# Kernel optimization log

Measured on AMD Instinct MI355X. Metric: run time of the kernel, lower is better.

## Reference

```python
import jax, jax.numpy as jnp
import numpy as np

NUM_NODES = 100000
NUM_EDGES = 1600000
NUM_GRAPHS = 64
NUM_FEATURES = 128
DIM = 128
OUTPUT_SIZE = 16


def setup_inputs() -> dict:
    key = jax.random.key(0)
    ks = jax.random.split(key, 7)
    features = jax.random.normal(ks[0], (NUM_NODES, NUM_FEATURES), dtype=jnp.float32)
    W1 = jax.random.normal(ks[1], (NUM_FEATURES, DIM), dtype=jnp.float32) / np.sqrt(NUM_FEATURES)
    W2 = jax.random.normal(ks[2], (DIM, DIM), dtype=jnp.float32) / np.sqrt(DIM)
    W3 = jax.random.normal(ks[3], (DIM, OUTPUT_SIZE), dtype=jnp.float32) / np.sqrt(DIM)
    src = jax.random.randint(ks[4], (NUM_EDGES,), 0, NUM_NODES, dtype=jnp.int32)
    dst = jax.random.randint(ks[5], (NUM_EDGES,), 0, NUM_NODES, dtype=jnp.int32)
    graph_ids = jnp.sort(jax.random.randint(ks[6], (NUM_NODES,), 0, NUM_GRAPHS, dtype=jnp.int32))
    return {"features": features, "W1": W1, "W2": W2, "W3": W3,
            "src": src, "dst": dst, "graph_ids": graph_ids}


def _graph_conv(x, W, src, dst, num_nodes):
    # DGL GraphConv, norm='none', bias=False: h_v = sum_{u -> v} (x_u @ W)
    xw = x @ W                      # [N, dim]
    msg = xw[src]                   # gather per edge [E, dim]
    return jax.ops.segment_sum(msg, dst, num_segments=num_nodes)


def reference(features, W1, W2, W3, src, dst, graph_ids):
    n = features.shape[0]
    h = jax.nn.relu(_graph_conv(features, W1, src, dst, n))  # conv1 + ReLU
    h = _graph_conv(h, W2, src, dst, n)                      # conv2
    # dgl.mean_nodes: per-graph mean over nodes
    sums = jax.ops.segment_sum(h, graph_ids, num_segments=NUM_GRAPHS)          # [G, dim]
    counts = jax.ops.segment_sum(jnp.ones((n,), h.dtype), graph_ids,
                                 num_segments=NUM_GRAPHS)                       # [G]
    pooled = sums / jnp.maximum(counts, 1.0)[:, None]
    out = pooled @ W3                                         # fc1 (no bias)
    return jax.nn.sigmoid(out)                                # torch.sigmoid activation
```

## Files before the change

### kernel.cpp

```cpp
#include <hip/hip_runtime.h>

#define FNX 4
#define CSLOT 32
#define OVCAP 65536
#define AP_CHUNK 32
#define AP_GBINS 8

typedef short bf16x8 __attribute__((ext_vector_type(8)));
typedef float f32x4  __attribute__((ext_vector_type(4)));

union U4S8 { uint4 u; bf16x8 s; };

__device__ __forceinline__ unsigned int f2bf(float f) {
    unsigned int u = __float_as_uint(f);
    return (u + 0x7fffu + ((u >> 16) & 1u)) >> 16;
}

__device__ __forceinline__ f32x4 nt_ld_f4(const float4* p) {
    return __builtin_nontemporal_load((const f32x4*)p);
}

__device__ __forceinline__ unsigned int enc_u8(float f) {
    return (unsigned int)fminf(fmaxf(f + 0.5f, 0.f), 255.9f);
}

__global__ __launch_bounds__(256) void fconv(
    const float4* __restrict__ F4, uint4* __restrict__ B4, int n16)
{
    int t = blockIdx.x * 256 + threadIdx.x;
    if (t >= n16) return;
    f32x4 a = nt_ld_f4(&F4[4 * t + 0]);
    f32x4 b = nt_ld_f4(&F4[4 * t + 1]);
    f32x4 c = nt_ld_f4(&F4[4 * t + 2]);
    f32x4 d = nt_ld_f4(&F4[4 * t + 3]);
    uint4 o;
    #define P4(v) (enc_u8(v.x * 16.f + 128.f) | (enc_u8(v.y * 16.f + 128.f) << 8) | \
                   (enc_u8(v.z * 16.f + 128.f) << 16) | (enc_u8(v.w * 16.f + 128.f) << 24))
    o.x = P4(a); o.y = P4(b); o.z = P4(c); o.w = P4(d);
    #undef P4
    B4[t] = o;
}

__global__ __launch_bounds__(256) void fillfix_xcd(
    const int* __restrict__ src, const int* __restrict__ dst,
    int* __restrict__ cnt, int* __restrict__ col,
    int* __restrict__ ovd, int* __restrict__ ovs, int* __restrict__ ov_cnt,
    int E, int N)
{
    int x  = blockIdx.x & (FNX - 1);
    int bi = blockIdx.x >> 2;
    int K  = gridDim.x >> 2;
    int chunk = (N + FNX - 1) / FNX;
    int lo = x * chunk;
    int hi = lo + chunk; if (hi > N) hi = N;
    for (int e = bi * 256 + threadIdx.x; e < E; e += K * 256) {
        int d = dst[e];
        if (d >= lo && d < hi) {
            int s = src[e];
            int pos = atomicAdd(&cnt[d], 1);
            if (pos < CSLOT) {
                col[(size_t)d * CSLOT + pos] = s;
            } else {
                int op = atomicAdd(ov_cnt, 1);
                if (op < OVCAP) { ovd[op] = d; ovs[op] = s; }
            }
        }
    }
}

#define ACC16(u) { \
    a0  += (float)((u).x & 0xffu);         a1  += (float)(((u).x >> 8) & 0xffu); \
    a2  += (float)(((u).x >> 16) & 0xffu); a3  += (float)((u).x >> 24); \
    a4  += (float)((u).y & 0xffu);         a5  += (float)(((u).y >> 8) & 0xffu); \
    a6  += (float)(((u).y >> 16) & 0xffu); a7  += (float)((u).y >> 24); \
    a8  += (float)((u).z & 0xffu);         a9  += (float)(((u).z >> 8) & 0xffu); \
    a10 += (float)(((u).z >> 16) & 0xffu); a11 += (float)((u).z >> 24); \
    a12 += (float)((u).w & 0xffu);         a13 += (float)(((u).w >> 8) & 0xffu); \
    a14 += (float)(((u).w >> 16) & 0xffu); a15 += (float)((u).w >> 24); }

#define GATHER8(SRCARR) { \
    int4 ca = *(const int4*)(cb + i); \
    int4 cd = *(const int4*)(cb + i + 4); \
    uint4 x0 = SRCARR[(size_t)ca.x * 8 + lane]; \
    uint4 x1 = SRCARR[(size_t)ca.y * 8 + lane]; \
    uint4 x2 = SRCARR[(size_t)ca.z * 8 + lane]; \
    uint4 x3 = SRCARR[(size_t)ca.w * 8 + lane]; \
    uint4 x4 = SRCARR[(size_t)cd.x * 8 + lane]; \
    uint4 x5 = SRCARR[(size_t)cd.y * 8 + lane]; \
    uint4 x6 = SRCARR[(size_t)cd.z * 8 + lane]; \
    uint4 x7 = SRCARR[(size_t)cd.w * 8 + lane]; \
    ACC16(x0) ACC16(x1) ACC16(x2) ACC16(x3) \
    ACC16(x4) ACC16(x5) ACC16(x6) ACC16(x7) }

#define GATHER4(SRCARR) { \
    int4 ca = *(const int4*)(cb + i); \
    uint4 x0 = SRCARR[(size_t)ca.x * 8 + lane]; \
    uint4 x1 = SRCARR[(size_t)ca.y * 8 + lane]; \
    uint4 x2 = SRCARR[(size_t)ca.z * 8 + lane]; \
    uint4 x3 = SRCARR[(size_t)ca.w * 8 + lane]; \
    ACC16(x0) ACC16(x1) ACC16(x2) ACC16(x3) }

__global__ __launch_bounds__(256) void csr_agg_u8(
    const uint4* __restrict__ X, const int* __restrict__ cnt,
    const int* __restrict__ col,
    const int* __restrict__ ovd, const int* __restrict__ ovs,
    const int* __restrict__ ov_cnt,
    uint4* __restrict__ T, int N)
{
    int v = blockIdx.x * 32 + (threadIdx.x >> 3);
    if (v >= N) return;
    int lane = threadIdx.x & 7;
    int c = cnt[v];
    int end = c < CSLOT ? c : CSLOT;
    const int* cb = col + (size_t)v * CSLOT;
    float a0=0,a1=0,a2=0,a3=0,a4=0,a5=0,a6=0,a7=0;
    float a8=0,a9=0,a10=0,a11=0,a12=0,a13=0,a14=0,a15=0;
    int i = 0;
    for (; i + 7 < end; i += 8) GATHER8(X)
    for (; i + 3 < end; i += 4) GATHER4(X)
    for (; i < end; ++i) {
        uint4 x0 = X[(size_t)cb[i] * 8 + lane];
        ACC16(x0)
    }
    int ntm = end;
    int oc = *ov_cnt; if (oc > OVCAP) oc = OVCAP;
    for (int k = 0; k < oc; ++k) {
        if (ovd[k] == v) {
            uint4 x0 = X[(size_t)ovs[k] * 8 + lane];
            ACC16(x0)
            ++ntm;
        }
    }
    float adj = 128.f * (float)ntm;
    #define CV(aa) f2bf((aa - adj) * 0.0625f)
    uint4 o1, o2;
    o1.x = CV(a0)  | (CV(a1)  << 16); o1.y = CV(a2)  | (CV(a3)  << 16);
    o1.z = CV(a4)  | (CV(a5)  << 16); o1.w = CV(a6)  | (CV(a7)  << 16);
    o2.x = CV(a8)  | (CV(a9)  << 16); o2.y = CV(a10) | (CV(a11) << 16);
    o2.z = CV(a12) | (CV(a13) << 16); o2.w = CV(a14) | (CV(a15) << 16);
    #undef CV
    T[(size_t)v * 16 + lane * 2 + 0] = o1;
    T[(size_t)v * 16 + lane * 2 + 1] = o2;
}

__global__ __launch_bounds__(256) void gemm_mfma(
    const uint4* __restrict__ T, const float* __restrict__ W,
    uint2* __restrict__ Y2u, int N, int RB)
{
    __shared__ char sWT[32768];
    __shared__ unsigned char sTu[4][16 * 128];
    int t = threadIdx.x;
    {
        int c = t & 127;
        int xo = (c & 7) << 4;
        #pragma unroll
        for (int i = 0; i < 8; ++i) {
            int kc = (t >> 7) + 2 * i;
            int k0 = kc * 8;
            unsigned int h[8];
            #pragma unroll
            for (int j = 0; j < 8; ++j)
                h[j] = f2bf(W[(k0 + j) * 128 + c]);
            uint4 pk;
            pk.x = h[0] | (h[1] << 16);
            pk.y = h[2] | (h[3] << 16);
            pk.z = h[4] | (h[5] << 16);
            pk.w = h[6] | (h[7] << 16);
            *(uint4*)(sWT + c * 256 + ((k0 * 2) ^ xo)) = pk;
        }
    }
    __syncthreads();

    int wid = t >> 6, l = t & 63;
    int rb = blockIdx.x * 4 + wid;
    if (rb >= RB) return;
    int lrow = l & 15, lg = l >> 4;
    int row = rb * 16 + lrow;

    U4S8 cv;
    bf16x8 a[4];
    #pragma unroll
    for (int kk = 0; kk < 4; ++kk) {
        cv.u = (row < N) ? T[(size_t)row * 16 + kk * 4 + lg] : make_uint4(0,0,0,0);
        a[kk] = cv.s;
    }

    f32x4 acc[8];
    #pragma unroll
    for (int ct = 0; ct < 8; ++ct) acc[ct] = (f32x4){0.f,0.f,0.f,0.f};

    #pragma unroll
    for (int ct = 0; ct < 8; ++ct) {
        int c = ct * 16 + lrow;
        const char* base = sWT + c * 256;
        int xo = (c & 7) << 4;
        #pragma unroll
        for (int kk = 0; kk < 4; ++kk) {
            cv.u = *(const uint4*)(base + ((kk * 64 + lg * 16) ^ xo));
            acc[ct] = __builtin_amdgcn_mfma_f32_16x16x32_bf16(a[kk], cv.s, acc[ct], 0, 0, 0);
        }
    }

    unsigned char* st = sTu[wid];
    #pragma unroll
    for (int ct = 0; ct < 8; ++ct) {
        #pragma unroll
        for (int r4 = 0; r4 < 4; ++r4)
            st[(lg * 4 + r4) * 128 + ct * 16 + lrow] =
                (unsigned char)enc_u8(acc[ct][r4] * 8.f);
    }
    #pragma unroll
    for (int r = 0; r < 4; ++r) {
        int rr = r * 4 + lg;
        uint2 q = *(const uint2*)(st + rr * 128 + lrow * 8);
        Y2u[((size_t)rb * 16 + rr) * 16 + lrow] = q;
    }
}

__global__ __launch_bounds__(256) void agg2pool(
    const uint4* __restrict__ Y2q, const int* __restrict__ cnt,
    const int* __restrict__ col,
    const int* __restrict__ ovd, const int* __restrict__ ovs,
    const int* __restrict__ ov_cnt, const int* __restrict__ gid,
    float* __restrict__ pooled, int N)
{
    __shared__ float sp[AP_GBINS * 128];
    int t = threadIdx.x;
    int v0 = blockIdx.x * AP_CHUNK;
    if (v0 >= N) return;
    int v1 = v0 + AP_CHUNK; if (v1 > N) v1 = N;
    int gLo = gid[v0];
    int gHi = gid[v1 - 1];
    bool fits = (gHi - gLo) < AP_GBINS;
    #pragma unroll
    for (int i = t; i < AP_GBINS * 128; i += 256) sp[i] = 0.f;
    __syncthreads();

    int lane = t & 7;
    int v = v0 + (t >> 3);
    if (v < v1) {
        int c = cnt[v];
        int end = c < CSLOT ? c : CSLOT;
        const int* cb = col + (size_t)v * CSLOT;
        float a0=0,a1=0,a2=0,a3=0,a4=0,a5=0,a6=0,a7=0;
        float a8=0,a9=0,a10=0,a11=0,a12=0,a13=0,a14=0,a15=0;
        int i = 0;
        for (; i + 7 < end; i += 8) GATHER8(Y2q)
        for (; i + 3 < end; i += 4) GATHER4(Y2q)
        for (; i < end; ++i) {
            uint4 y0 = Y2q[(size_t)cb[i] * 8 + lane];
            ACC16(y0)
        }
        int oc = *ov_cnt; if (oc > OVCAP) oc = OVCAP;
        for (int k = 0; k < oc; ++k) {
            if (ovd[k] == v) {
                uint4 y0 = Y2q[(size_t)ovs[k] * 8 + lane];
                ACC16(y0)
            }
        }
        if (fits) {
            float* b = &sp[(gid[v] - gLo) * 128 + lane * 16];
            atomicAdd(&b[0],  a0);  atomicAdd(&b[1],  a1);
            atomicAdd(&b[2],  a2);  atomicAdd(&b[3],  a3);
            atomicAdd(&b[4],  a4);  atomicAdd(&b[5],  a5);
            atomicAdd(&b[6],  a6);  atomicAdd(&b[7],  a7);
            atomicAdd(&b[8],  a8);  atomicAdd(&b[9],  a9);
            atomicAdd(&b[10], a10); atomicAdd(&b[11], a11);
            atomicAdd(&b[12], a12); atomicAdd(&b[13], a13);
            atomicAdd(&b[14], a14); atomicAdd(&b[15], a15);
        } else {
            float* b = &pooled[gid[v] * 128 + lane * 16];
            unsafeAtomicAdd(&b[0],  a0  * 0.125f); unsafeAtomicAdd(&b[1],  a1  * 0.125f);
            unsafeAtomicAdd(&b[2],  a2  * 0.125f); unsafeAtomicAdd(&b[3],  a3  * 0.125f);
            unsafeAtomicAdd(&b[4],  a4  * 0.125f); unsafeAtomicAdd(&b[5],  a5  * 0.125f);
            unsafeAtomicAdd(&b[6],  a6  * 0.125f); unsafeAtomicAdd(&b[7],  a7  * 0.125f);
            unsafeAtomicAdd(&b[8],  a8  * 0.125f); unsafeAtomicAdd(&b[9],  a9  * 0.125f);
            unsafeAtomicAdd(&b[10], a10 * 0.125f); unsafeAtomicAdd(&b[11], a11 * 0.125f);
            unsafeAtomicAdd(&b[12], a12 * 0.125f); unsafeAtomicAdd(&b[13], a13 * 0.125f);
            unsafeAtomicAdd(&b[14], a14 * 0.125f); unsafeAtomicAdd(&b[15], a15 * 0.125f);
        }
    }
    __syncthreads();

    if (fits) {
        int nb = (gHi - gLo + 1) * 128;
        for (int i = t; i < nb; i += 256)
            unsafeAtomicAdd(&pooled[gLo * 128 + i], sp[i] * 0.125f);
    }
}

__global__ __launch_bounds__(1024) void final_fused(
    const float* __restrict__ pooled, const int* __restrict__ gid, int N,
    const float* __restrict__ W2, const float* __restrict__ W3,
    float* __restrict__ out)
{
    __shared__ float sW23[128 * 16];
    __shared__ int lb[65];
    int t = threadIdx.x;
    if (t <= 64) {
        int lo = 0, hi = N;
        while (lo < hi) { int mid = (lo + hi) >> 1; if (gid[mid] < t) lo = mid + 1; else hi = mid; }
        lb[t] = lo;
    }
    for (int idx = t; idx < 2048; idx += 1024) {
        int k = idx >> 4, o = idx & 15;
        float a = 0.f;
        #pragma unroll 16
        for (int jj = 0; jj < 128; ++jj)
            a += W2[k * 128 + jj] * W3[jj * 16 + o];
        sW23[idx] = a;
    }
    __syncthreads();
    int g = t >> 4, o = t & 15;
    float cntf = fmaxf((float)(lb[g + 1] - lb[g]), 1.0f);
    float acc = 0.f;
    #pragma unroll 16
    for (int k = 0; k < 128; ++k)
        acc += pooled[g * 128 + k] * sW23[k * 16 + o];
    acc /= cntf;
    out[g * 16 + o] = 1.0f / (1.0f + __expf(-acc));
}

extern "C" void kernel_launch(void* const* d_in, const int* in_sizes, int n_in,
                              void* d_out, int out_size, void* d_ws, size_t ws_size,
                              hipStream_t stream)
{
    const float* features = (const float*)d_in[0];
    const float* W1       = (const float*)d_in[1];
    const float* W2       = (const float*)d_in[2];
    const float* W3       = (const float*)d_in[3];
    const int*   src      = (const int*)d_in[4];
    const int*   dst      = (const int*)d_in[5];
    const int*   gid      = (const int*)d_in[6];
    int N = in_sizes[0] / 128;
    int E = in_sizes[4];
    float* out = (float*)d_out;

    int RB = (N + 15) / 16;

    char* ws = (char*)d_ws;
    size_t p = 0;
    auto alloc = [&](size_t bytes) { void* r = ws + p; p = (p + bytes + 255) & ~(size_t)255; return r; };
    unsigned int* fbu  = (unsigned int*)alloc((size_t)N * 128);
    unsigned int* tbf  = (unsigned int*)alloc((size_t)N * 128 * 2);
    uint2*        Y2u  = (uint2*)alloc((size_t)RB * 16 * 128);
    int*   col    = (int*)alloc((size_t)N * CSLOT * sizeof(int));
    int*   ovd    = (int*)alloc((size_t)OVCAP * sizeof(int));
    int*   ovs    = (int*)alloc((size_t)OVCAP * sizeof(int));
    size_t cntB = (((size_t)N * 4) + 255) & ~(size_t)255;
    char*  zr   = (char*)alloc(cntB + 256 + 64 * 128 * 4);
    int*   cnt    = (int*)zr;
    int*   ov_cnt = (int*)(zr + cntB);
    float* pooled = (float*)(zr + cntB + 256);

    int n16      = N * 8;
    int aggGrid  = (N + 31) / 32;
    int fillGrid = 2048;
    int gGrid    = (RB + 3) / 4;
    int apGrid   = (N + AP_CHUNK - 1) / AP_CHUNK;

    fconv<<<(n16 + 255) / 256, 256, 0, stream>>>((const float4*)features, (uint4*)fbu, n16);

    (void)hipMemsetAsync(zr, 0, cntB + 256 + 64 * 128 * 4, stream);
    fillfix_xcd<<<fillGrid, 256, 0, stream>>>(src, dst, cnt, col, ovd, ovs, ov_cnt, E, N);

    csr_agg_u8<<<aggGrid, 256, 0, stream>>>((const uint4*)fbu, cnt, col, ovd, ovs, ov_cnt, (uint4*)tbf, N);
    gemm_mfma<<<gGrid, 256, 0, stream>>>((const uint4*)tbf, W1, Y2u, N, RB);

    agg2pool<<<apGrid, 256, 0, stream>>>((const uint4*)Y2u, cnt, col, ovd, ovs, ov_cnt, gid, pooled, N);

    final_fused<<<1, 1024, 0, stream>>>(pooled, gid, N, W2, W3, out);
}
```

Measured before the change: 281.3 us.

## Process two nodes per thread group in gather-aggregation kernels for more memory-level parallelism

Both the first-layer CSR aggregation and the fused second aggregation+pool kernel now assign two destination nodes to each 8-lane group, interleaving their neighbor gathers so 16 independent row loads are in flight. Block coverage doubles to 64 nodes, halving the grid, and launch bounds request 4 blocks per CU. This aims to hide gather latency and, in the pool kernel, amortise the shared-memory bin setup over more nodes. The cost is doubled accumulator registers, fewer blocks, and overflow-list scans run per node.

```diff
diff --git a/kernel.cpp b/kernel.cpp
--- a/kernel.cpp
+++ b/kernel.cpp
@@ -3,7 +3,7 @@
 #define FNX 4
 #define CSLOT 32
 #define OVCAP 65536
-#define AP_CHUNK 32
+#define AP_CHUNK 64
 #define AP_GBINS 8
 
 typedef short bf16x8 __attribute__((ext_vector_type(8)));
@@ -68,17 +68,43 @@
     }
 }
 
-#define ACC16(u) { \
-    a0  += (float)((u).x & 0xffu);         a1  += (float)(((u).x >> 8) & 0xffu); \
-    a2  += (float)(((u).x >> 16) & 0xffu); a3  += (float)((u).x >> 24); \
-    a4  += (float)((u).y & 0xffu);         a5  += (float)(((u).y >> 8) & 0xffu); \
-    a6  += (float)(((u).y >> 16) & 0xffu); a7  += (float)((u).y >> 24); \
-    a8  += (float)((u).z & 0xffu);         a9  += (float)(((u).z >> 8) & 0xffu); \
-    a10 += (float)(((u).z >> 16) & 0xffu); a11 += (float)((u).z >> 24); \
-    a12 += (float)((u).w & 0xffu);         a13 += (float)(((u).w >> 8) & 0xffu); \
-    a14 += (float)(((u).w >> 16) & 0xffu); a15 += (float)((u).w >> 24); }
-
-#define GATHER8(SRCARR) { \
+#define ACC16(u, q) { \
+    q[0]  += (float)((u).x & 0xffu);         q[1]  += (float)(((u).x >> 8) & 0xffu); \
+    q[2]  += (float)(((u).x >> 16) & 0xffu); q[3]  += (float)((u).x >> 24); \
+    q[4]  += (float)((u).y & 0xffu);         q[5]  += (float)(((u).y >> 8) & 0xffu); \
+    q[6]  += (float)(((u).y >> 16) & 0xffu); q[7]  += (float)((u).y >> 24); \
+    q[8]  += (float)((u).z & 0xffu);         q[9]  += (float)(((u).z >> 8) & 0xffu); \
+    q[10] += (float)(((u).z >> 16) & 0xffu); q[11] += (float)((u).z >> 24); \
+    q[12] += (float)(((u).w & 0xffu));       q[13] += (float)(((u).w >> 8) & 0xffu); \
+    q[14] += (float)(((u).w >> 16) & 0xffu); q[15] += (float)((u).w >> 24); }
+
+#define DUAL8(SRCARR, cbA, iA, qA, cbB, iB, qB) { \
+    int4 pa0 = *(const int4*)(cbA + iA); \
+    int4 pa1 = *(const int4*)(cbA + iA + 4); \
+    int4 pb0 = *(const int4*)(cbB + iB); \
+    int4 pb1 = *(const int4*)(cbB + iB + 4); \
+    uint4 xA0 = SRCARR[(size_t)pa0.x * 8 + lane]; \
+    uint4 xA1 = SRCARR[(size_t)pa0.y * 8 + lane]; \
+    uint4 xA2 = SRCARR[(size_t)pa0.z * 8 + lane]; \
+    uint4 xA3 = SRCARR[(size_t)pa0.w * 8 + lane]; \
+    uint4 xA4 = SRCARR[(size_t)pa1.x * 8 + lane]; \
+    uint4 xA5 = SRCARR[(size_t)pa1.y * 8 + lane]; \
+    uint4 xA6 = SRCARR[(size_t)pa1.z * 8 + lane]; \
+    uint4 xA7 = SRCARR[(size_t)pa1.w * 8 + lane]; \
+    uint4 xB0 = SRCARR[(size_t)pb0.x * 8 + lane]; \
+    uint4 xB1 = SRCARR[(size_t)pb0.y * 8 + lane]; \
+    uint4 xB2 = SRCARR[(size_t)pb0.z * 8 + lane]; \
+    uint4 xB3 = SRCARR[(size_t)pb0.w * 8 + lane]; \
+    uint4 xB4 = SRCARR[(size_t)pb1.x * 8 + lane]; \
+    uint4 xB5 = SRCARR[(size_t)pb1.y * 8 + lane]; \
+    uint4 xB6 = SRCARR[(size_t)pb1.z * 8 + lane]; \
+    uint4 xB7 = SRCARR[(size_t)pb1.w * 8 + lane]; \
+    ACC16(xA0, qA) ACC16(xA1, qA) ACC16(xA2, qA) ACC16(xA3, qA) \
+    ACC16(xA4, qA) ACC16(xA5, qA) ACC16(xA6, qA) ACC16(xA7, qA) \
+    ACC16(xB0, qB) ACC16(xB1, qB) ACC16(xB2, qB) ACC16(xB3, qB) \
+    ACC16(xB4, qB) ACC16(xB5, qB) ACC16(xB6, qB) ACC16(xB7, qB) }
+
+#define GATHER8(SRCARR, cb, i, q) { \
     int4 ca = *(const int4*)(cb + i); \
     int4 cd = *(const int4*)(cb + i + 4); \
     uint4 x0 = SRCARR[(size_t)ca.x * 8 + lane]; \
@@ -89,58 +115,96 @@
     uint4 x5 = SRCARR[(size_t)cd.y * 8 + lane]; \
     uint4 x6 = SRCARR[(size_t)cd.z * 8 + lane]; \
     uint4 x7 = SRCARR[(size_t)cd.w * 8 + lane]; \
-    ACC16(x0) ACC16(x1) ACC16(x2) ACC16(x3) \
-    ACC16(x4) ACC16(x5) ACC16(x6) ACC16(x7) }
-
-#define GATHER4(SRCARR) { \
+    ACC16(x0, q) ACC16(x1, q) ACC16(x2, q) ACC16(x3, q) \
+    ACC16(x4, q) ACC16(x5, q) ACC16(x6, q) ACC16(x7, q) }
+
+#define GATHER4(SRCARR, cb, i, q) { \
     int4 ca = *(const int4*)(cb + i); \
     uint4 x0 = SRCARR[(size_t)ca.x * 8 + lane]; \
     uint4 x1 = SRCARR[(size_t)ca.y * 8 + lane]; \
     uint4 x2 = SRCARR[(size_t)ca.z * 8 + lane]; \
     uint4 x3 = SRCARR[(size_t)ca.w * 8 + lane]; \
-    ACC16(x0) ACC16(x1) ACC16(x2) ACC16(x3) }
-
-__global__ __launch_bounds__(256) void csr_agg_u8(
+    ACC16(x0, q) ACC16(x1, q) ACC16(x2, q) ACC16(x3, q) }
+
+#define TAIL_OV(SRCARR, cb, i, endq, v, q) { \
+    for (; i + 3 < endq; i += 4) GATHER4(SRCARR, cb, i, q) \
+    for (; i < endq; ++i) { \
+        uint4 x0 = SRCARR[(size_t)cb[i] * 8 + lane]; \
+        ACC16(x0, q) \
+    } \
+    for (int k = 0; k < oc; ++k) { \
+        if (ovd[k] == v) { \
+            uint4 x0 = SRCARR[(size_t)ovs[k] * 8 + lane]; \
+            ACC16(x0, q) \
+        } \
+    } }
+
+__global__ __launch_bounds__(256, 4) void csr_agg_u8(
     const uint4* __restrict__ X, const int* __restrict__ cnt,
     const int* __restrict__ col,
     const int* __restrict__ ovd, const int* __restrict__ ovs,
     const int* __restrict__ ov_cnt,
     uint4* __restrict__ T, int N)
 {
-    int v = blockIdx.x * 32 + (threadIdx.x >> 3);
-    if (v >= N) return;
+    int v0 = blockIdx.x * 64;
+    int nid = threadIdx.x >> 3;
     int lane = threadIdx.x & 7;
-    int c = cnt[v];
-    int end = c < CSLOT ? c : CSLOT;
-    const int* cb = col + (size_t)v * CSLOT;
-    float a0=0,a1=0,a2=0,a3=0,a4=0,a5=0,a6=0,a7=0;
-    float a8=0,a9=0,a10=0,a11=0,a12=0,a13=0,a14=0,a15=0;
-    int i = 0;
-    for (; i + 7 < end; i += 8) GATHER8(X)
-    for (; i + 3 < end; i += 4) GATHER4(X)
-    for (; i < end; ++i) {
-        uint4 x0 = X[(size_t)cb[i] * 8 + lane];
-        ACC16(x0)
-    }
-    int ntm = end;
+    int vA = v0 + nid, vB = v0 + nid + 32;
     int oc = *ov_cnt; if (oc > OVCAP) oc = OVCAP;
-    for (int k = 0; k < oc; ++k) {
-        if (ovd[k] == v) {
-            uint4 x0 = X[(size_t)ovs[k] * 8 + lane];
-            ACC16(x0)
-            ++ntm;
-        }
-    }
-    float adj = 128.f * (float)ntm;
-    #define CV(aa) f2bf((aa - adj) * 0.0625f)
-    uint4 o1, o2;
-    o1.x = CV(a0)  | (CV(a1)  << 16); o1.y = CV(a2)  | (CV(a3)  << 16);
-    o1.z = CV(a4)  | (CV(a5)  << 16); o1.w = CV(a6)  | (CV(a7)  << 16);
-    o2.x = CV(a8)  | (CV(a9)  << 16); o2.y = CV(a10) | (CV(a11) << 16);
-    o2.z = CV(a12) | (CV(a13) << 16); o2.w = CV(a14) | (CV(a15) << 16);
+
+    int endA = 0, endB = 0;
+    if (vA < N) { int c = cnt[vA]; endA = c < CSLOT ? c : CSLOT; }
+    if (vB < N) { int c = cnt[vB]; endB = c < CSLOT ? c : CSLOT; }
+    const int* cbA = col + (size_t)vA * CSLOT;
+    const int* cbB = col + (size_t)vB * CSLOT;
+
+    float qA[16], qB[16];
+    #pragma unroll
+    for (int k = 0; k < 16; ++k) { qA[k] = 0.f; qB[k] = 0.f; }
+
+    int iA = 0, iB = 0;
+    while (iA + 7 < endA && iB + 7 < endB) {
+        DUAL8(X, cbA, iA, qA, cbB, iB, qB)
+        iA += 8; iB += 8;
+    }
+    for (; iA + 7 < endA; iA += 8) GATHER8(X, cbA, iA, qA)
+    for (; iB + 7 < endB; iB += 8) GATHER8(X, cbB, iB, qB)
+    int ntmA = endA, ntmB = endB;
+    if (vA < N) {
+        int preA = 0;
+        for (int k = 0; k < oc; ++k) if (ovd[k] == vA) ++preA;
+        ntmA += preA;
+    }
+    if (vB < N) {
+        int preB = 0;
+        for (int k = 0; k < oc; ++k) if (ovd[k] == vB) ++preB;
+        ntmB += preB;
+    }
+    TAIL_OV(X, cbA, iA, endA, vA, qA)
+    TAIL_OV(X, cbB, iB, endB, vB, qB)
+
+    #define CV(aa, adj) f2bf(((aa) - (adj)) * 0.0625f)
+    if (vA < N) {
+        float adj = 128.f * (float)ntmA;
+        uint4 o1, o2;
+        o1.x = CV(qA[0],adj)  | (CV(qA[1],adj)  << 16); o1.y = CV(qA[2],adj)  | (CV(qA[3],adj)  << 16);
+        o1.z = CV(qA[4],adj)  | (CV(qA[5],adj)  << 16); o1.w = CV(qA[6],adj)  | (CV(qA[7],adj)  << 16);
+        o2.x = CV(qA[8],adj)  | (CV(qA[9],adj)  << 16); o2.y = CV(qA[10],adj) | (CV(qA[11],adj) << 16);
+        o2.z = CV(qA[12],adj) | (CV(qA[13],adj) << 16); o2.w = CV(qA[14],adj) | (CV(qA[15],adj) << 16);
+        T[(size_t)vA * 16 + lane * 2 + 0] = o1;
+        T[(size_t)vA * 16 + lane * 2 + 1] = o2;
+    }
+    if (vB < N) {
+        float adj = 128.f * (float)ntmB;
+        uint4 o1, o2;
+        o1.x = CV(qB[0],adj)  | (CV(qB[1],adj)  << 16); o1.y = CV(qB[2],adj)  | (CV(qB[3],adj)  << 16);
+        o1.z = CV(qB[4],adj)  | (CV(qB[5],adj)  << 16); o1.w = CV(qB[6],adj)  | (CV(qB[7],adj)  << 16);
+        o2.x = CV(qB[8],adj)  | (CV(qB[9],adj)  << 16); o2.y = CV(qB[10],adj) | (CV(qB[11],adj) << 16);
+        o2.z = CV(qB[12],adj) | (CV(qB[13],adj) << 16); o2.w = CV(qB[14],adj) | (CV(qB[15],adj) << 16);
+        T[(size_t)vB * 16 + lane * 2 + 0] = o1;
+        T[(size_t)vB * 16 + lane * 2 + 1] = o2;
+    }
     #undef CV
-    T[(size_t)v * 16 + lane * 2 + 0] = o1;
-    T[(size_t)v * 16 + lane * 2 + 1] = o2;
 }
 
 __global__ __launch_bounds__(256) void gemm_mfma(
@@ -217,7 +281,7 @@
     }
 }
 
-__global__ __launch_bounds__(256) void agg2pool(
+__global__ __launch_bounds__(256, 4) void agg2pool(
     const uint4* __restrict__ Y2q, const int* __restrict__ cnt,
     const int* __restrict__ col,
     const int* __restrict__ ovd, const int* __restrict__ ovs,
@@ -236,50 +300,44 @@
     for (int i = t; i < AP_GBINS * 128; i += 256) sp[i] = 0.f;
     __syncthreads();
 
+    int nid = t >> 3;
     int lane = t & 7;
-    int v = v0 + (t >> 3);
-    if (v < v1) {
-        int c = cnt[v];
-        int end = c < CSLOT ? c : CSLOT;
-        const int* cb = col + (size_t)v * CSLOT;
-        float a0=0,a1=0,a2=0,a3=0,a4=0,a5=0,a6=0,a7=0;
-        float a8=0,a9=0,a10=0,a11=0,a12=0,a13=0,a14=0,a15=0;
-        int i = 0;
-        for (; i + 7 < end; i += 8) GATHER8(Y2q)
-        for (; i + 3 < end; i += 4) GATHER4(Y2q)
-        for (; i < end; ++i) {
-            uint4 y0 = Y2q[(size_t)cb[i] * 8 + lane];
-            ACC16(y0)
-        }
-        int oc = *ov_cnt; if (oc > OVCAP) oc = OVCAP;
-        for (int k = 0; k < oc; ++k) {
-            if (ovd[k] == v) {
-                uint4 y0 = Y2q[(size_t)ovs[k] * 8 + lane];
-                ACC16(y0)
-            }
-        }
-        if (fits) {
-            float* b = &sp[(gid[v] - gLo) * 128 + lane * 16];
-            atomicAdd(&b[0],  a0);  atomicAdd(&b[1],  a1);
-            atomicAdd(&b[2],  a2);  atomicAdd(&b[3],  a3);
-            atomicAdd(&b[4],  a4);  atomicAdd(&b[5],  a5);
-            atomicAdd(&b[6],  a6);  atomicAdd(&b[7],  a7);
-            atomicAdd(&b[8],  a8);  atomicAdd(&b[9],  a9);
-            atomicAdd(&b[10], a10); atomicAdd(&b[11], a11);
-            atomicAdd(&b[12], a12); atomicAdd(&b[13], a13);
-            atomicAdd(&b[14], a14); atomicAdd(&b[15], a15);
-        } else {
-            float* b = &pooled[gid[v] * 128 + lane * 16];
-            unsafeAtomicAdd(&b[0],  a0  * 0.125f); unsafeAtomicAdd(&b[1],  a1  * 0.125f);
-            unsafeAtomicAdd(&b[2],  a2  * 0.125f); unsafeAtomicAdd(&b[3],  a3  * 0.125f);
-            unsafeAtomicAdd(&b[4],  a4  * 0.125f); unsafeAtomicAdd(&b[5],  a5  * 0.125f);
-            unsafeAtomicAdd(&b[6],  a6  * 0.125f); unsafeAtomicAdd(&b[7],  a7  * 0.125f);
-            unsafeAtomicAdd(&b[8],  a8  * 0.125f); unsafeAtomicAdd(&b[9],  a9  * 0.125f);
-            unsafeAtomicAdd(&b[10], a10 * 0.125f); unsafeAtomicAdd(&b[11], a11 * 0.125f);
-            unsafeAtomicAdd(&b[12], a12 * 0.125f); unsafeAtomicAdd(&b[13], a13 * 0.125f);
-            unsafeAtomicAdd(&b[14], a14 * 0.125f); unsafeAtomicAdd(&b[15], a15 * 0.125f);
-        }
-    }
+    int vA = v0 + nid, vB = v0 + nid + 32;
+    int oc = *ov_cnt; if (oc > OVCAP) oc = OVCAP;
+
+    int endA = 0, endB = 0;
+    if (vA < v1) { int c = cnt[vA]; endA = c < CSLOT ? c : CSLOT; }
+    if (vB < v1) { int c = cnt[vB]; endB = c < CSLOT ? c : CSLOT; }
+    const int* cbA = col + (size_t)vA * CSLOT;
+    const int* cbB = col + (size_t)vB * CSLOT;
+
+    float qA[16], qB[16];
+    #pragma unroll
+    for (int k = 0; k < 16; ++k) { qA[k] = 0.f; qB[k] = 0.f; }
+
+    int iA = 0, iB = 0;
+    while (iA + 7 < endA && iB + 7 < endB) {
+        DUAL8(Y2q, cbA, iA, qA, cbB, iB, qB)
+        iA += 8; iB += 8;
+    }
+    for (; iA + 7 < endA; iA += 8) GATHER8(Y2q, cbA, iA, qA)
+    for (; iB + 7 < endB; iB += 8) GATHER8(Y2q, cbB, iB, qB)
+    TAIL_OV(Y2q, cbA, iA, endA, vA, qA)
+    TAIL_OV(Y2q, cbB, iB, endB, vB, qB)
+
+    #define FLUSH(v, q) if (v < v1) { \
+        if (fits) { \
+            float* b = &sp[(gid[v] - gLo) * 128 + lane * 16]; \
+            _Pragma("unroll") \
+            for (int k = 0; k < 16; ++k) atomicAdd(&b[k], q[k]); \
+        } else { \
+            float* b = &pooled[gid[v] * 128 + lane * 16]; \
+            _Pragma("unroll") \
+            for (int k = 0; k < 16; ++k) unsafeAtomicAdd(&b[k], q[k] * 0.125f); \
+        } }
+    FLUSH(vA, qA)
+    FLUSH(vB, qB)
+    #undef FLUSH
     __syncthreads();
 
     if (fits) {
@@ -354,7 +412,7 @@
     float* pooled = (float*)(zr + cntB + 256);
 
     int n16      = N * 8;
-    int aggGrid  = (N + 31) / 32;
+    int aggGrid  = (N + 63) / 64;
     int fillGrid = 2048;
     int gGrid    = (RB + 3) / 4;
     int apGrid   = (N + AP_CHUNK - 1) / AP_CHUNK;
```

New measurement: 300.1 us. +6.7%, slower.
